# Performance work log

Measured on AMD Instinct MI355X. Metric: run time of the kernel, lower is better.

Reference implementation:

```python
import math
import jax, jax.numpy as jnp
import numpy as np

B, S, D, H = 2, 2048, 1024, 16
HD = D // H  # head_dim = 64
LN_EPS = 1e-5


def setup_inputs() -> dict:
    key = jax.random.key(0)
    ks = jax.random.split(key, 12)
    scale = 1.0 / math.sqrt(D)
    inp = {
        "x": jax.random.normal(ks[0], (B, S, D), dtype=jnp.float32),
        "cdr_mask": jax.random.uniform(ks[1], (B, 1, S, S), dtype=jnp.float32),
        "Wq": jax.random.normal(ks[2], (D, D), dtype=jnp.float32) * scale,
        "bq": jnp.zeros((D,), dtype=jnp.float32),
        "Wk": jax.random.normal(ks[3], (D, D), dtype=jnp.float32) * scale,
        "bk": jnp.zeros((D,), dtype=jnp.float32),
        "Wv": jax.random.normal(ks[4], (D, D), dtype=jnp.float32) * scale,
        "bv": jnp.zeros((D,), dtype=jnp.float32),
        "Wo": jax.random.normal(ks[5], (D, D), dtype=jnp.float32) * scale,
        "bo": jnp.zeros((D,), dtype=jnp.float32),
        "gamma": jnp.ones((D,), dtype=jnp.float32),
        "beta": jnp.zeros((D,), dtype=jnp.float32),
        "cdr_weight": jnp.float32(1.0),
    }
    return inp


def _rotate_half(t):
    # even / odd interleaved halves, as in the torch module
    t1 = t[..., ::2]
    t2 = t[..., 1::2]
    return jnp.stack((-t2, t1), axis=-1).reshape(t.shape)


def reference(x, cdr_mask, Wq, bq, Wk, bk, Wv, bv, Wo, bo, gamma, beta, cdr_weight):
    b, s, d = x.shape
    # RoPE tables (concatenated, NOT interleaved -- faithful to source)
    inv_freq = 1.0 / (10000.0 ** (jnp.arange(0, HD, 2, dtype=jnp.float32) / HD))
    pos = jnp.arange(s, dtype=jnp.float32)
    sinusoid = pos[:, None] * inv_freq[None, :]          # [S, HD/2]
    sin_pos = jnp.concatenate([jnp.sin(sinusoid)] * 2, axis=-1)[None, None]  # [1,1,S,HD]
    cos_pos = jnp.concatenate([jnp.cos(sinusoid)] * 2, axis=-1)[None, None]

    def proj(W, bias):
        return (x @ W.T + bias).reshape(b, s, H, HD).transpose(0, 2, 1, 3)  # [B,H,S,HD]

    Q = proj(Wq, bq)
    K = proj(Wk, bk)
    V = proj(Wv, bv)
    Q = Q * cos_pos + _rotate_half(Q) * sin_pos
    K = K * cos_pos + _rotate_half(K) * sin_pos

    scores = jnp.einsum('bhqd,bhkd->bhqk', Q, K) / math.sqrt(HD)
    scores = scores + cdr_mask * cdr_weight
    probs = jax.nn.softmax(scores, axis=-1)
    attn = jnp.einsum('bhqk,bhkd->bhqd', probs, V)       # [B,H,S,HD]
    attn = attn.transpose(0, 2, 1, 3).reshape(b, s, d)
    out = attn @ Wo.T + bo                               # dropout is identity at eval

    y = x + out
    mu = jnp.mean(y, axis=-1, keepdims=True)
    var = jnp.var(y, axis=-1, keepdims=True)
    return (y - mu) / jnp.sqrt(var + LN_EPS) * gamma + beta
```

## Files before the change

kernel.cpp:

```cpp
#include <hip/hip_runtime.h>
#include <hip/hip_bf16.h>
#include <math.h>

#define Bn  2
#define Sn  2048
#define Dn  1024
#define Hn  16
#define HDn 64

typedef __attribute__((ext_vector_type(8))) short bf16x8;
typedef __attribute__((ext_vector_type(4))) short bf16x4;
typedef __attribute__((ext_vector_type(4))) float f32x4;

#define LOG2E 1.44269504088896340736f

__device__ __forceinline__ float fexp2(float x) {
    return __builtin_amdgcn_exp2f(x);
}

__device__ __forceinline__ uint2 pack4bf(float a, float b, float c, float d) {
    union { __hip_bfloat162 h2[2]; uint2 u; } p;
    p.h2[0] = __float22bfloat162_rn(make_float2(a, b));
    p.h2[1] = __float22bfloat162_rn(make_float2(c, d));
    return p.u;
}

__device__ __forceinline__ bf16x4 pack4bfv(float a, float b, float c, float d) {
    union { __hip_bfloat162 h2[2]; bf16x4 v; } p;
    p.h2[0] = __float22bfloat162_rn(make_float2(a, b));
    p.h2[1] = __float22bfloat162_rn(make_float2(c, d));
    return p.v;
}

__device__ __forceinline__ void g2l16(const __hip_bfloat16* g, __hip_bfloat16* lbase) {
    __builtin_amdgcn_global_load_lds(
        (const __attribute__((address_space(1))) void*)g,
        (__attribute__((address_space(3))) void*)lbase, 16, 0, 0);
}

__global__ __launch_bounds__(256) void prep_kernel(
    const float* __restrict__ x,
    const float* __restrict__ Wq, const float* __restrict__ Wk,
    const float* __restrict__ Wv, const float* __restrict__ Wo,
    const float* __restrict__ mask, const float* __restrict__ cwp,
    __hip_bfloat16* __restrict__ Xb,
    __hip_bfloat16* __restrict__ Wqb, __hip_bfloat16* __restrict__ Wkb,
    __hip_bfloat16* __restrict__ Wvb, __hip_bfloat16* __restrict__ Wob,
    __hip_bfloat16* __restrict__ Mw)
{
    const int bx = blockIdx.x, tid = threadIdx.x;
    if (bx < 4096) {
        const size_t i = (size_t)bx * 1024 + tid * 4;
        float4 v = *(const float4*)(x + i);
        *(uint2*)(Xb + i) = pack4bf(v.x, v.y, v.z, v.w);
    } else if (bx < 8192) {
        const int r = bx - 4096;
        const int which = r >> 10;
        const size_t i = (size_t)(r & 1023) * 1024 + tid * 4;
        const float* s = (which == 0) ? Wq : (which == 1) ? Wk : (which == 2) ? Wv : Wo;
        __hip_bfloat16* d = (which == 0) ? Wqb : (which == 1) ? Wkb : (which == 2) ? Wvb : Wob;
        float4 v = *(const float4*)(s + i);
        *(uint2*)(d + i) = pack4bf(v.x, v.y, v.z, v.w);
    } else {
        const size_t i = (size_t)(bx - 8192) * 1024 + tid * 4;
        const float cw = cwp[0] * LOG2E;
        float4 v = *(const float4*)(mask + i);
        *(uint2*)(Mw + i) = pack4bf(v.x * cw, v.y * cw, v.z * cw, v.w * cw);
    }
}

__global__ __launch_bounds__(256) void qkv_proj(
    const __hip_bfloat16* __restrict__ X,
    const __hip_bfloat16* __restrict__ Wqb, const __hip_bfloat16* __restrict__ Wkb,
    const __hip_bfloat16* __restrict__ Wvb,
    const float* __restrict__ bq, const float* __restrict__ bk,
    const float* __restrict__ bv,
    __hip_bfloat16* __restrict__ Qo, __hip_bfloat16* __restrict__ Ko,
    __hip_bfloat16* __restrict__ Vo)
{
    __shared__ __hip_bfloat16 Xs[128 * 32];
    __shared__ __hip_bfloat16 Ws[128 * 32];
    const int tid  = threadIdx.x;
    const int w    = tid >> 6, lane = tid & 63;
    const int lrow = lane & 15, lhi = lane >> 4;
    const int pj   = blockIdx.x >> 3;
    const int m0   = blockIdx.y * 128, n0 = (blockIdx.x & 7) * 128;
    const int rm   = (w & 1) * 64;
    const int rn   = (w >> 1) * 64;
    const int srow = lane >> 2, cb = lane & 3;

    const __hip_bfloat16* Wb  = (pj == 0) ? Wqb : (pj == 1) ? Wkb : Wvb;
    const float*          bias = (pj == 0) ? bq : (pj == 1) ? bk : bv;

    f32x4 acc[16];
#pragma unroll
    for (int i = 0; i < 16; i++) acc[i] = (f32x4){0.f, 0.f, 0.f, 0.f};

    for (int k0 = 0; k0 < Dn; k0 += 32) {
#pragma unroll
        for (int j = 0; j < 2; j++) {
            const int row = w * 32 + j * 16 + srow;
            const int sc  = (cb ^ ((row >> 1) & 3)) << 3;
            g2l16(X  + (size_t)(m0 + row) * Dn + k0 + sc, &Xs[(w * 32 + j * 16) * 32]);
            g2l16(Wb + (size_t)(n0 + row) * Dn + k0 + sc, &Ws[(w * 32 + j * 16) * 32]);
        }
        __syncthreads();

        bf16x8 FX[4], FW[4];
#pragma unroll
        for (int t = 0; t < 4; t++) {
            const int ra = rm + t * 16 + lrow;
            FX[t] = *(const bf16x8*)&Xs[ra * 32 + ((lhi ^ ((ra >> 1) & 3)) << 3)];
            const int rb = rn + t * 16 + lrow;
            FW[t] = *(const bf16x8*)&Ws[rb * 32 + ((lhi ^ ((rb >> 1) & 3)) << 3)];
        }
        if (pj == 2) {
#pragma unroll
            for (int tm = 0; tm < 4; tm++)
#pragma unroll
                for (int tn = 0; tn < 4; tn++)
                    acc[tm * 4 + tn] = __builtin_amdgcn_mfma_f32_16x16x32_bf16(
                        FX[tm], FW[tn], acc[tm * 4 + tn], 0, 0, 0);
        } else {
#pragma unroll
            for (int tn = 0; tn < 4; tn++)
#pragma unroll
                for (int tm = 0; tm < 4; tm++)
                    acc[tn * 4 + tm] = __builtin_amdgcn_mfma_f32_16x16x32_bf16(
                        FW[tn], FX[tm], acc[tn * 4 + tm], 0, 0, 0);
        }
        __syncthreads();
    }

    const int h = (n0 >> 6) + (w >> 1);

    if (pj != 2) {
        __hip_bfloat16* outb = (pj == 0) ? Qo : Ko;
        const float NEG_L2C = -0.41524101186092033f;
        const float SCL = 0.125f * LOG2E;
#pragma unroll
        for (int tn = 0; tn < 4; tn++) {
            const int hd0 = tn * 16 + lhi * 4;
            const float4 b4 = *(const float4*)&bias[n0 + rn + hd0];
            const float f0 = exp2f((float)((hd0 + 0) & 31) * NEG_L2C);
            const float f1 = exp2f((float)((hd0 + 1) & 31) * NEG_L2C);
            const float f2 = exp2f((float)((hd0 + 2) & 31) * NEG_L2C);
            const float f3 = exp2f((float)((hd0 + 3) & 31) * NEG_L2C);
#pragma unroll
            for (int tm = 0; tm < 4; tm++) {
                const int m = m0 + rm + tm * 16 + lrow;
                const int s = m & (Sn - 1), bb = m >> 11;
                f32x4 a = acc[tn * 4 + tm];
                float v0 = a[0] + b4.x, v1 = a[1] + b4.y;
                float v2 = a[2] + b4.z, v3 = a[3] + b4.w;
                if (pj == 0) { v0 *= SCL; v1 *= SCL; v2 *= SCL; v3 *= SCL; }
                const float sf = (float)s;
                const float c0 = __cosf(sf * f0), c1 = __cosf(sf * f1);
                const float c2 = __cosf(sf * f2), c3 = __cosf(sf * f3);
                const float s0 = __sinf(sf * f0), s1 = __sinf(sf * f1);
                const float s2 = __sinf(sf * f2), s3 = __sinf(sf * f3);
                const float r0 = v0 * c0 - v1 * s0;
                const float r1 = v1 * c1 + v0 * s1;
                const float r2 = v2 * c2 - v3 * s2;
                const float r3 = v3 * c3 + v2 * s3;
                *(uint2*)(outb + ((size_t)(bb * Hn + h) * Sn + s) * HDn + hd0) =
                    pack4bf(r0, r1, r2, r3);
            }
        }
    } else {
#pragma unroll
        for (int tn = 0; tn < 4; tn++) {
            const int c = tn * 16 + lrow;
            const float bc = bias[n0 + rn + c];
#pragma unroll
            for (int tm = 0; tm < 4; tm++) {
                const int mb = m0 + rm + tm * 16 + lhi * 4;
                const int s = mb & (Sn - 1), bb = mb >> 11;
                f32x4 a = acc[tm * 4 + tn];
                *(uint2*)(Vo + ((size_t)(bb * Hn + h) * HDn + c) * Sn + s) =
                    pack4bf(a[0] + bc, a[1] + bc, a[2] + bc, a[3] + bc);
            }
        }
    }
}

__global__ __launch_bounds__(256) void o_proj(
    const __hip_bfloat16* __restrict__ X,
    const __hip_bfloat16* __restrict__ Wb,
    const float* __restrict__ bias,
    const float* __restrict__ resid,
    float* __restrict__ outf)
{
    __shared__ __hip_bfloat16 Xs[128 * 32];
    __shared__ __hip_bfloat16 Ws[128 * 32];
    const int tid  = threadIdx.x;
    const int w    = tid >> 6, lane = tid & 63;
    const int lrow = lane & 15, lhi = lane >> 4;
    const int m0   = blockIdx.y * 128, n0 = blockIdx.x * 128;
    const int rm   = (w & 1) * 64;
    const int rn   = (w >> 1) * 64;
    const int srow = lane >> 2, cb = lane & 3;

    f32x4 acc[16];
#pragma unroll
    for (int i = 0; i < 16; i++) acc[i] = (f32x4){0.f, 0.f, 0.f, 0.f};

    for (int k0 = 0; k0 < Dn; k0 += 32) {
#pragma unroll
        for (int j = 0; j < 2; j++) {
            const int row = w * 32 + j * 16 + srow;
            const int sc  = (cb ^ ((row >> 1) & 3)) << 3;
            g2l16(X  + (size_t)(m0 + row) * Dn + k0 + sc, &Xs[(w * 32 + j * 16) * 32]);
            g2l16(Wb + (size_t)(n0 + row) * Dn + k0 + sc, &Ws[(w * 32 + j * 16) * 32]);
        }
        __syncthreads();

        bf16x8 FX[4], FW[4];
#pragma unroll
        for (int t = 0; t < 4; t++) {
            const int ra = rm + t * 16 + lrow;
            FX[t] = *(const bf16x8*)&Xs[ra * 32 + ((lhi ^ ((ra >> 1) & 3)) << 3)];
            const int rb = rn + t * 16 + lrow;
            FW[t] = *(const bf16x8*)&Ws[rb * 32 + ((lhi ^ ((rb >> 1) & 3)) << 3)];
        }
#pragma unroll
        for (int tn = 0; tn < 4; tn++)
#pragma unroll
            for (int tm = 0; tm < 4; tm++)
                acc[tn * 4 + tm] = __builtin_amdgcn_mfma_f32_16x16x32_bf16(
                    FW[tn], FX[tm], acc[tn * 4 + tm], 0, 0, 0);
        __syncthreads();
    }

#pragma unroll
    for (int tn = 0; tn < 4; tn++) {
        const int nb = n0 + rn + tn * 16 + lhi * 4;
        const float4 b4 = *(const float4*)&bias[nb];
#pragma unroll
        for (int tm = 0; tm < 4; tm++) {
            const int m = m0 + rm + tm * 16 + lrow;
            f32x4 a = acc[tn * 4 + tm];
            const float4 rr = *(const float4*)&resid[(size_t)m * Dn + nb];
            *(float4*)(outf + (size_t)m * Dn + nb) =
                make_float4(a[0] + b4.x + rr.x, a[1] + b4.y + rr.y,
                            a[2] + b4.z + rr.z, a[3] + b4.w + rr.w);
        }
    }
}

struct __align__(16) TileBuf {
    __hip_bfloat16 K[64 * 64];
    __hip_bfloat16 V[64 * 64];
    __hip_bfloat16 M[64 * 64];
};

__device__ __forceinline__ void stage_tiles(
    TileBuf& t,
    const __hip_bfloat16* __restrict__ Kb,
    const __hip_bfloat16* __restrict__ Vb,
    const __hip_bfloat16* __restrict__ Mq0,
    int k0, int w, int lane)
{
#pragma unroll
    for (int j = 0; j < 2; j++) {
        const int row = w * 16 + j * 8 + (lane >> 3);
        const int blk = (lane & 7) ^ (row & 7);
        g2l16(Kb + (size_t)(k0 + row) * HDn + blk * 8, &t.K[(w * 16 + j * 8) * 64]);
        g2l16(Vb + (size_t)row * Sn + k0 + blk * 8,    &t.V[(w * 16 + j * 8) * 64]);
        g2l16(Mq0 + (size_t)row * Sn + k0 + blk * 8,   &t.M[(w * 16 + j * 8) * 64]);
    }
}

__global__ __launch_bounds__(256) void attn_kernel(
    const __hip_bfloat16* __restrict__ Q,
    const __hip_bfloat16* __restrict__ K,
    const __hip_bfloat16* __restrict__ Vt,
    const __hip_bfloat16* __restrict__ Mw,
    __hip_bfloat16* __restrict__ A)
{
    __shared__ TileBuf tb[2];
    const int tid  = threadIdx.x;
    const int w    = tid >> 6, lane = tid & 63;
    const int lrow = lane & 15, lhi = lane >> 4;
    const int bh   = blockIdx.y, b = bh >> 4, h = bh & 15;
    const int q0   = blockIdx.x * 64;
    const int q    = q0 + w * 16 + lrow;

    const __hip_bfloat16* Qp  = Q + ((size_t)bh * Sn + q) * HDn + lhi * 8;
    const bf16x8 Qf0 = *(const bf16x8*)(Qp);
    const bf16x8 Qf1 = *(const bf16x8*)(Qp + 32);
    const __hip_bfloat16* Kb  = K  + (size_t)bh * Sn * HDn;
    const __hip_bfloat16* Vb  = Vt + (size_t)bh * HDn * Sn;
    const __hip_bfloat16* Mq0 = Mw + ((size_t)b * Sn + q0) * Sn;

    f32x4 Oc[4];
#pragma unroll
    for (int i = 0; i < 4; i++) Oc[i] = (f32x4){0.f, 0.f, 0.f, 0.f};
    float lsum = 0.f;

    stage_tiles(tb[0], Kb, Vb, Mq0, 0, w, lane);
    __syncthreads();

    for (int it = 0; it < Sn / 64; it++) {
        const int k0 = it * 64;
        if (it + 1 < Sn / 64)
            stage_tiles(tb[(it + 1) & 1], Kb, Vb, Mq0, k0 + 64, w, lane);
        const TileBuf& t = tb[it & 1];

        f32x4 st[4];
#pragma unroll
        for (int kt = 0; kt < 4; kt++) {
            const int rl = kt * 16 + lrow;
            const bf16x8 ka = *(const bf16x8*)&t.K[rl * 64 + ((lhi       ^ (rl & 7)) * 8)];
            const bf16x8 kc = *(const bf16x8*)&t.K[rl * 64 + (((4 + lhi) ^ (rl & 7)) * 8)];
            f32x4 z = (f32x4){0.f, 0.f, 0.f, 0.f};
            z = __builtin_amdgcn_mfma_f32_16x16x32_bf16(ka, Qf0, z, 0, 0, 0);
            z = __builtin_amdgcn_mfma_f32_16x16x32_bf16(kc, Qf1, z, 0, 0, 0);
            st[kt] = z;
        }

        const int rq = w * 16 + lrow;
        bf16x4 pk[4];
#pragma unroll
        for (int kt = 0; kt < 4; kt++) {
            const int eo = (((2 * kt + (lhi >> 1)) ^ (rq & 7)) * 8) + (lhi & 1) * 4;
            union { uint2 u; __hip_bfloat16 hh[4]; } mu;
            mu.u = *(const uint2*)&t.M[rq * 64 + eo];
            const float p0 = fexp2(st[kt][0] + __bfloat162float(mu.hh[0]));
            const float p1 = fexp2(st[kt][1] + __bfloat162float(mu.hh[1]));
            const float p2 = fexp2(st[kt][2] + __bfloat162float(mu.hh[2]));
            const float p3 = fexp2(st[kt][3] + __bfloat162float(mu.hh[3]));
            lsum += (p0 + p1) + (p2 + p3);
            pk[kt] = pack4bfv(p0, p1, p2, p3);
        }

#pragma unroll
        for (int ch = 0; ch < 4; ch++) {
            const int rv = ch * 16 + lrow;
#pragma unroll
            for (int kt = 0; kt < 4; kt++) {
                const int eo = (((2 * kt + (lhi >> 1)) ^ (rv & 7)) * 8) + (lhi & 1) * 4;
                const bf16x4 vf = *(const bf16x4*)&t.V[rv * 64 + eo];
                Oc[ch] = __builtin_amdgcn_mfma_f32_16x16x16bf16_1k(
                    vf, pk[kt], Oc[ch], 0, 0, 0);
            }
        }
        __syncthreads();
    }

    lsum += __shfl_xor(lsum, 16, 64);
    lsum += __shfl_xor(lsum, 32, 64);
    const float inv = 1.f / lsum;

    __hip_bfloat16* ap = A + ((size_t)(b * Sn + q)) * Dn + h * HDn;
#pragma unroll
    for (int ch = 0; ch < 4; ch++) {
        *(uint2*)(ap + ch * 16 + lhi * 4) =
            pack4bf(Oc[ch][0] * inv, Oc[ch][1] * inv, Oc[ch][2] * inv, Oc[ch][3] * inv);
    }
}

__global__ __launch_bounds__(256) void ln_kernel(
    const float* __restrict__ Yin, const float* __restrict__ gamma,
    const float* __restrict__ beta, float* __restrict__ out)
{
    __shared__ float2 wred[4];
    const int m   = blockIdx.x;
    const int tid = threadIdx.x;
    const size_t base = (size_t)m * Dn + tid * 4;
    float4 y = *(const float4*)(Yin + base);

    float s1 = y.x + y.y + y.z + y.w;
    float s2 = y.x * y.x + y.y * y.y + y.z * y.z + y.w * y.w;
#pragma unroll
    for (int off = 32; off; off >>= 1) {
        s1 += __shfl_xor(s1, off, 64);
        s2 += __shfl_xor(s2, off, 64);
    }
    if ((tid & 63) == 0) wred[tid >> 6] = make_float2(s1, s2);
    __syncthreads();
    const float S1 = wred[0].x + wred[1].x + wred[2].x + wred[3].x;
    const float S2 = wred[0].y + wred[1].y + wred[2].y + wred[3].y;
    const float mu  = S1 * (1.f / Dn);
    const float var = S2 * (1.f / Dn) - mu * mu;
    const float rin = rsqrtf(var + 1e-5f);

    float4 gv = *(const float4*)(gamma + tid * 4);
    float4 bv = *(const float4*)(beta  + tid * 4);
    *(float4*)(out + base) = make_float4((y.x - mu) * rin * gv.x + bv.x,
                                         (y.y - mu) * rin * gv.y + bv.y,
                                         (y.z - mu) * rin * gv.z + bv.z,
                                         (y.w - mu) * rin * gv.w + bv.w);
}

extern "C" void kernel_launch(void* const* d_in, const int* in_sizes, int n_in,
                              void* d_out, int out_size, void* d_ws, size_t ws_size,
                              hipStream_t stream)
{
    const float* x     = (const float*)d_in[0];
    const float* mask  = (const float*)d_in[1];
    const float* Wq    = (const float*)d_in[2];
    const float* bq    = (const float*)d_in[3];
    const float* Wk    = (const float*)d_in[4];
    const float* bk    = (const float*)d_in[5];
    const float* Wv    = (const float*)d_in[6];
    const float* bv    = (const float*)d_in[7];
    const float* Wo    = (const float*)d_in[8];
    const float* bo    = (const float*)d_in[9];
    const float* gamma = (const float*)d_in[10];
    const float* beta  = (const float*)d_in[11];
    const float* cw    = (const float*)d_in[12];
    float* out = (float*)d_out;

    const size_t MB = 1024 * 1024;
    char* ws = (char*)d_ws;
    __hip_bfloat16* Xb  = (__hip_bfloat16*)(ws);
    __hip_bfloat16* Qb  = (__hip_bfloat16*)(ws +  8 * MB);
    __hip_bfloat16* Kb  = (__hip_bfloat16*)(ws + 16 * MB);
    __hip_bfloat16* Vtb = (__hip_bfloat16*)(ws + 24 * MB);
    __hip_bfloat16* Mw  = (__hip_bfloat16*)(ws + 32 * MB);
    __hip_bfloat16* Wqb = (__hip_bfloat16*)(ws + 48 * MB);
    __hip_bfloat16* Wkb = (__hip_bfloat16*)(ws + 50 * MB);
    __hip_bfloat16* Wvb = (__hip_bfloat16*)(ws + 52 * MB);
    __hip_bfloat16* Wob = (__hip_bfloat16*)(ws + 54 * MB);
    __hip_bfloat16* Ab  = Xb;

    prep_kernel<<<16384, 256, 0, stream>>>(x, Wq, Wk, Wv, Wo, mask, cw,
                                           Xb, Wqb, Wkb, Wvb, Wob, Mw);
    qkv_proj<<<dim3(24, 32), 256, 0, stream>>>(Xb, Wqb, Wkb, Wvb,
                                               bq, bk, bv, Qb, Kb, Vtb);
    attn_kernel<<<dim3(Sn / 64, Bn * Hn), 256, 0, stream>>>(Qb, Kb, Vtb, Mw, Ab);
    o_proj<<<dim3(8, 32), 256, 0, stream>>>(Ab, Wob, bo, x, out);
    ln_kernel<<<Bn * Sn, 256, 0, stream>>>(out, gamma, beta, out);
}
```

Baseline: 292.2 us.

## Read fp32 mask directly in attention and double-buffer GEMM LDS tiles

Drops the prep pass that converted and pre-scaled the attention mask to bf16. The attention kernel now streams the fp32 mask into LDS and applies the cdr_weight·log2e scale with an fma before the exp2. This removes one full read-plus-write pass over the mask, but each attention block now loads twice as many mask bytes from L2/LLC and uses more LDS per block, which may lower occupancy. Separately, the QKV and output projection GEMMs get double-buffered LDS tiles so the next k-slice is loaded while the current one is multiplied.

```diff
diff --git a/kernel.cpp b/kernel.cpp
--- a/kernel.cpp
+++ b/kernel.cpp
@@ -32,7 +32,7 @@
     return p.v;
 }
 
-__device__ __forceinline__ void g2l16(const __hip_bfloat16* g, __hip_bfloat16* lbase) {
+__device__ __forceinline__ void g2l16(const void* g, void* lbase) {
     __builtin_amdgcn_global_load_lds(
         (const __attribute__((address_space(1))) void*)g,
         (__attribute__((address_space(3))) void*)lbase, 16, 0, 0);
@@ -42,18 +42,16 @@
     const float* __restrict__ x,
     const float* __restrict__ Wq, const float* __restrict__ Wk,
     const float* __restrict__ Wv, const float* __restrict__ Wo,
-    const float* __restrict__ mask, const float* __restrict__ cwp,
     __hip_bfloat16* __restrict__ Xb,
     __hip_bfloat16* __restrict__ Wqb, __hip_bfloat16* __restrict__ Wkb,
-    __hip_bfloat16* __restrict__ Wvb, __hip_bfloat16* __restrict__ Wob,
-    __hip_bfloat16* __restrict__ Mw)
+    __hip_bfloat16* __restrict__ Wvb, __hip_bfloat16* __restrict__ Wob)
 {
     const int bx = blockIdx.x, tid = threadIdx.x;
     if (bx < 4096) {
         const size_t i = (size_t)bx * 1024 + tid * 4;
         float4 v = *(const float4*)(x + i);
         *(uint2*)(Xb + i) = pack4bf(v.x, v.y, v.z, v.w);
-    } else if (bx < 8192) {
+    } else {
         const int r = bx - 4096;
         const int which = r >> 10;
         const size_t i = (size_t)(r & 1023) * 1024 + tid * 4;
@@ -61,11 +59,6 @@
         __hip_bfloat16* d = (which == 0) ? Wqb : (which == 1) ? Wkb : (which == 2) ? Wvb : Wob;
         float4 v = *(const float4*)(s + i);
         *(uint2*)(d + i) = pack4bf(v.x, v.y, v.z, v.w);
-    } else {
-        const size_t i = (size_t)(bx - 8192) * 1024 + tid * 4;
-        const float cw = cwp[0] * LOG2E;
-        float4 v = *(const float4*)(mask + i);
-        *(uint2*)(Mw + i) = pack4bf(v.x * cw, v.y * cw, v.z * cw, v.w * cw);
     }
 }
 
@@ -78,8 +71,8 @@
     __hip_bfloat16* __restrict__ Qo, __hip_bfloat16* __restrict__ Ko,
     __hip_bfloat16* __restrict__ Vo)
 {
-    __shared__ __hip_bfloat16 Xs[128 * 32];
-    __shared__ __hip_bfloat16 Ws[128 * 32];
+    __shared__ __hip_bfloat16 Xs[2][128 * 32];
+    __shared__ __hip_bfloat16 Ws[2][128 * 32];
     const int tid  = threadIdx.x;
     const int w    = tid >> 6, lane = tid & 63;
     const int lrow = lane & 15, lhi = lane >> 4;
@@ -89,30 +82,37 @@
     const int rn   = (w >> 1) * 64;
     const int srow = lane >> 2, cb = lane & 3;
 
-    const __hip_bfloat16* Wb  = (pj == 0) ? Wqb : (pj == 1) ? Wkb : Wvb;
+    const __hip_bfloat16* Wb   = (pj == 0) ? Wqb : (pj == 1) ? Wkb : Wvb;
     const float*          bias = (pj == 0) ? bq : (pj == 1) ? bk : bv;
 
     f32x4 acc[16];
 #pragma unroll
     for (int i = 0; i < 16; i++) acc[i] = (f32x4){0.f, 0.f, 0.f, 0.f};
 
-    for (int k0 = 0; k0 < Dn; k0 += 32) {
+    auto stage = [&](int bsel, int k0) {
 #pragma unroll
         for (int j = 0; j < 2; j++) {
             const int row = w * 32 + j * 16 + srow;
             const int sc  = (cb ^ ((row >> 1) & 3)) << 3;
-            g2l16(X  + (size_t)(m0 + row) * Dn + k0 + sc, &Xs[(w * 32 + j * 16) * 32]);
-            g2l16(Wb + (size_t)(n0 + row) * Dn + k0 + sc, &Ws[(w * 32 + j * 16) * 32]);
-        }
-        __syncthreads();
+            g2l16(X  + (size_t)(m0 + row) * Dn + k0 + sc, &Xs[bsel][(w * 32 + j * 16) * 32]);
+            g2l16(Wb + (size_t)(n0 + row) * Dn + k0 + sc, &Ws[bsel][(w * 32 + j * 16) * 32]);
+        }
+    };
+
+    stage(0, 0);
+    __syncthreads();
+
+    for (int it = 0; it < Dn / 32; it++) {
+        if (it + 1 < Dn / 32) stage((it + 1) & 1, (it + 1) * 32);
+        const int bs = it & 1;
 
         bf16x8 FX[4], FW[4];
 #pragma unroll
         for (int t = 0; t < 4; t++) {
             const int ra = rm + t * 16 + lrow;
-            FX[t] = *(const bf16x8*)&Xs[ra * 32 + ((lhi ^ ((ra >> 1) & 3)) << 3)];
+            FX[t] = *(const bf16x8*)&Xs[bs][ra * 32 + ((lhi ^ ((ra >> 1) & 3)) << 3)];
             const int rb = rn + t * 16 + lrow;
-            FW[t] = *(const bf16x8*)&Ws[rb * 32 + ((lhi ^ ((rb >> 1) & 3)) << 3)];
+            FW[t] = *(const bf16x8*)&Ws[bs][rb * 32 + ((lhi ^ ((rb >> 1) & 3)) << 3)];
         }
         if (pj == 2) {
 #pragma unroll
@@ -191,8 +191,8 @@
     const float* __restrict__ resid,
     float* __restrict__ outf)
 {
-    __shared__ __hip_bfloat16 Xs[128 * 32];
-    __shared__ __hip_bfloat16 Ws[128 * 32];
+    __shared__ __hip_bfloat16 Xs[2][128 * 32];
+    __shared__ __hip_bfloat16 Ws[2][128 * 32];
     const int tid  = threadIdx.x;
     const int w    = tid >> 6, lane = tid & 63;
     const int lrow = lane & 15, lhi = lane >> 4;
@@ -205,23 +205,30 @@
 #pragma unroll
     for (int i = 0; i < 16; i++) acc[i] = (f32x4){0.f, 0.f, 0.f, 0.f};
 
-    for (int k0 = 0; k0 < Dn; k0 += 32) {
+    auto stage = [&](int bsel, int k0) {
 #pragma unroll
         for (int j = 0; j < 2; j++) {
             const int row = w * 32 + j * 16 + srow;
             const int sc  = (cb ^ ((row >> 1) & 3)) << 3;
-            g2l16(X  + (size_t)(m0 + row) * Dn + k0 + sc, &Xs[(w * 32 + j * 16) * 32]);
-            g2l16(Wb + (size_t)(n0 + row) * Dn + k0 + sc, &Ws[(w * 32 + j * 16) * 32]);
-        }
-        __syncthreads();
+            g2l16(X  + (size_t)(m0 + row) * Dn + k0 + sc, &Xs[bsel][(w * 32 + j * 16) * 32]);
+            g2l16(Wb + (size_t)(n0 + row) * Dn + k0 + sc, &Ws[bsel][(w * 32 + j * 16) * 32]);
+        }
+    };
+
+    stage(0, 0);
+    __syncthreads();
+
+    for (int it = 0; it < Dn / 32; it++) {
+        if (it + 1 < Dn / 32) stage((it + 1) & 1, (it + 1) * 32);
+        const int bs = it & 1;
 
         bf16x8 FX[4], FW[4];
 #pragma unroll
         for (int t = 0; t < 4; t++) {
             const int ra = rm + t * 16 + lrow;
-            FX[t] = *(const bf16x8*)&Xs[ra * 32 + ((lhi ^ ((ra >> 1) & 3)) << 3)];
+            FX[t] = *(const bf16x8*)&Xs[bs][ra * 32 + ((lhi ^ ((ra >> 1) & 3)) << 3)];
             const int rb = rn + t * 16 + lrow;
-            FW[t] = *(const bf16x8*)&Ws[rb * 32 + ((lhi ^ ((rb >> 1) & 3)) << 3)];
+            FW[t] = *(const bf16x8*)&Ws[bs][rb * 32 + ((lhi ^ ((rb >> 1) & 3)) << 3)];
         }
 #pragma unroll
         for (int tn = 0; tn < 4; tn++)
@@ -251,14 +258,14 @@
 struct __align__(16) TileBuf {
     __hip_bfloat16 K[64 * 64];
     __hip_bfloat16 V[64 * 64];
-    __hip_bfloat16 M[64 * 64];
+    float          M[64 * 64];
 };
 
 __device__ __forceinline__ void stage_tiles(
     TileBuf& t,
     const __hip_bfloat16* __restrict__ Kb,
     const __hip_bfloat16* __restrict__ Vb,
-    const __hip_bfloat16* __restrict__ Mq0,
+    const float* __restrict__ Mq0,
     int k0, int w, int lane)
 {
 #pragma unroll
@@ -267,7 +274,12 @@
         const int blk = (lane & 7) ^ (row & 7);
         g2l16(Kb + (size_t)(k0 + row) * HDn + blk * 8, &t.K[(w * 16 + j * 8) * 64]);
         g2l16(Vb + (size_t)row * Sn + k0 + blk * 8,    &t.V[(w * 16 + j * 8) * 64]);
-        g2l16(Mq0 + (size_t)row * Sn + k0 + blk * 8,   &t.M[(w * 16 + j * 8) * 64]);
+    }
+#pragma unroll
+    for (int j = 0; j < 4; j++) {
+        const int row = w * 16 + j * 4 + (lane >> 4);
+        const int blk = (lane & 15) ^ (row & 7);
+        g2l16(Mq0 + (size_t)row * Sn + k0 + blk * 4,   &t.M[(w * 16 + j * 4) * 64]);
     }
 }
 
@@ -275,7 +287,8 @@
     const __hip_bfloat16* __restrict__ Q,
     const __hip_bfloat16* __restrict__ K,
     const __hip_bfloat16* __restrict__ Vt,
-    const __hip_bfloat16* __restrict__ Mw,
+    const float* __restrict__ mask,
+    const float* __restrict__ cwp,
     __hip_bfloat16* __restrict__ A)
 {
     __shared__ TileBuf tb[2];
@@ -285,13 +298,14 @@
     const int bh   = blockIdx.y, b = bh >> 4, h = bh & 15;
     const int q0   = blockIdx.x * 64;
     const int q    = q0 + w * 16 + lrow;
+    const float cwl = cwp[0] * LOG2E;
 
     const __hip_bfloat16* Qp  = Q + ((size_t)bh * Sn + q) * HDn + lhi * 8;
     const bf16x8 Qf0 = *(const bf16x8*)(Qp);
     const bf16x8 Qf1 = *(const bf16x8*)(Qp + 32);
     const __hip_bfloat16* Kb  = K  + (size_t)bh * Sn * HDn;
     const __hip_bfloat16* Vb  = Vt + (size_t)bh * HDn * Sn;
-    const __hip_bfloat16* Mq0 = Mw + ((size_t)b * Sn + q0) * Sn;
+    const float*          Mq0 = mask + ((size_t)b * Sn + q0) * Sn;
 
     f32x4 Oc[4];
 #pragma unroll
@@ -323,13 +337,12 @@
         bf16x4 pk[4];
 #pragma unroll
         for (int kt = 0; kt < 4; kt++) {
-            const int eo = (((2 * kt + (lhi >> 1)) ^ (rq & 7)) * 8) + (lhi & 1) * 4;
-            union { uint2 u; __hip_bfloat16 hh[4]; } mu;
-            mu.u = *(const uint2*)&t.M[rq * 64 + eo];
-            const float p0 = fexp2(st[kt][0] + __bfloat162float(mu.hh[0]));
-            const float p1 = fexp2(st[kt][1] + __bfloat162float(mu.hh[1]));
-            const float p2 = fexp2(st[kt][2] + __bfloat162float(mu.hh[2]));
-            const float p3 = fexp2(st[kt][3] + __bfloat162float(mu.hh[3]));
+            const int mb = (kt * 4 + lhi) ^ (rq & 7);
+            const f32x4 mf = *(const f32x4*)&t.M[rq * 64 + mb * 4];
+            const float p0 = fexp2(fmaf(mf[0], cwl, st[kt][0]));
+            const float p1 = fexp2(fmaf(mf[1], cwl, st[kt][1]));
+            const float p2 = fexp2(fmaf(mf[2], cwl, st[kt][2]));
+            const float p3 = fexp2(fmaf(mf[3], cwl, st[kt][3]));
             lsum += (p0 + p1) + (p2 + p3);
             pk[kt] = pack4bfv(p0, p1, p2, p3);
         }
@@ -418,18 +431,17 @@
     __hip_bfloat16* Qb  = (__hip_bfloat16*)(ws +  8 * MB);
     __hip_bfloat16* Kb  = (__hip_bfloat16*)(ws + 16 * MB);
     __hip_bfloat16* Vtb = (__hip_bfloat16*)(ws + 24 * MB);
-    __hip_bfloat16* Mw  = (__hip_bfloat16*)(ws + 32 * MB);
-    __hip_bfloat16* Wqb = (__hip_bfloat16*)(ws + 48 * MB);
-    __hip_bfloat16* Wkb = (__hip_bfloat16*)(ws + 50 * MB);
-    __hip_bfloat16* Wvb = (__hip_bfloat16*)(ws + 52 * MB);
-    __hip_bfloat16* Wob = (__hip_bfloat16*)(ws + 54 * MB);
+    __hip_bfloat16* Wqb = (__hip_bfloat16*)(ws + 32 * MB);
+    __hip_bfloat16* Wkb = (__hip_bfloat16*)(ws + 34 * MB);
+    __hip_bfloat16* Wvb = (__hip_bfloat16*)(ws + 36 * MB);
+    __hip_bfloat16* Wob = (__hip_bfloat16*)(ws + 38 * MB);
     __hip_bfloat16* Ab  = Xb;
 
-    prep_kernel<<<16384, 256, 0, stream>>>(x, Wq, Wk, Wv, Wo, mask, cw,
-                                           Xb, Wqb, Wkb, Wvb, Wob, Mw);
+    prep_kernel<<<8192, 256, 0, stream>>>(x, Wq, Wk, Wv, Wo,
+                                          Xb, Wqb, Wkb, Wvb, Wob);
     qkv_proj<<<dim3(24, 32), 256, 0, stream>>>(Xb, Wqb, Wkb, Wvb,
                                                bq, bk, bv, Qb, Kb, Vtb);
-    attn_kernel<<<dim3(Sn / 64, Bn * Hn), 256, 0, stream>>>(Qb, Kb, Vtb, Mw, Ab);
+    attn_kernel<<<dim3(Sn / 64, Bn * Hn), 256, 0, stream>>>(Qb, Kb, Vtb, mask, cw, Ab);
     o_proj<<<dim3(8, 32), 256, 0, stream>>>(Ab, Wob, bo, x, out);
     ln_kernel<<<Bn * Sn, 256, 0, stream>>>(out, gamma, beta, out);
 }
```

Result: slower. 303.6 us (+3.9%).
